# Kernel optimization log

Measured on AMD Instinct MI355X. Metric: run time of the kernel, lower is better.

The kernel has to match this reference:

```python
import jax, jax.numpy as jnp
import numpy as np

C = 256
CQK = C // 8  # query/key channels


def setup_inputs() -> dict:
    key = jax.random.key(0)
    ks = jax.random.split(key, 7)
    B, H, W = 4, 64, 64
    x = jax.random.normal(ks[0], (B, C, H, W), dtype=jnp.float32)
    # 1x1 conv weights stored as [out_ch, in_ch] (kernel spatial dims are 1)
    sc = 1.0 / np.sqrt(C)
    Wq = jax.random.uniform(ks[1], (CQK, C), jnp.float32, -sc, sc)
    bq = jax.random.uniform(ks[2], (CQK,), jnp.float32, -sc, sc)
    Wk = jax.random.uniform(ks[3], (CQK, C), jnp.float32, -sc, sc)
    bk = jax.random.uniform(ks[4], (CQK,), jnp.float32, -sc, sc)
    Wv = jax.random.uniform(ks[5], (C, C), jnp.float32, -sc, sc)
    bv = jax.random.uniform(ks[6], (C,), jnp.float32, -sc, sc)
    gamma = jnp.zeros((1,), dtype=jnp.float32)
    return {"x": x, "Wq": Wq, "bq": bq, "Wk": Wk, "bk": bk, "Wv": Wv, "bv": bv, "gamma": gamma}


def reference(x, Wq, bq, Wk, bk, Wv, bv, gamma):
    B, Ch, H, W = x.shape
    N = H * W
    xf = x.reshape(B, Ch, N)  # [B, C, N]
    # 1x1 convs == per-pixel linear projections
    q = jnp.einsum('oc,bcn->bno', Wq, xf) + bq  # [B, N, CQK]
    k = jnp.einsum('oc,bcn->bon', Wk, xf) + bk[None, :, None]  # [B, CQK, N]
    v = jnp.einsum('oc,bcn->bon', Wv, xf) + bv[None, :, None]  # [B, C, N]
    s = jnp.einsum('bnd,bdm->bnm', q, k)  # [B, N, N]
    attn = jax.nn.softmax(s, axis=-1)
    # out[b,c,i] = sum_j v[b,c,j] * attn[b,i,j]
    out = jnp.einsum('bcj,bij->bci', v, attn).reshape(B, Ch, H, W)
    return x + gamma[0] * out
```

## Files before the change

### kernel.cpp

```cpp
#include <hip/hip_runtime.h>
#include <math.h>

#define BATCH 4
#define CCH   256
#define DQK   32
#define NPIX  4096
#define LOG2E 1.44269504088896340736f

typedef __attribute__((ext_vector_type(8)))  short          short8_t;
typedef __attribute__((ext_vector_type(4)))  unsigned short ushort4_t;
typedef __attribute__((ext_vector_type(8)))  unsigned short ushort8_t;
typedef __attribute__((ext_vector_type(16))) float          f32x16;
typedef __attribute__((ext_vector_type(2)))  unsigned int   uint2_t;

#if __has_builtin(__builtin_amdgcn_exp2f)
#define EXP2F(x) __builtin_amdgcn_exp2f(x)
#else
#define EXP2F(x) exp2f(x)
#endif

#define MFMA32(a, b, c) __builtin_amdgcn_mfma_f32_32x32x16_bf16(a, b, c, 0, 0, 0)

static __device__ __forceinline__ unsigned short f2bf(float f) {
    union { float f; unsigned int u; } v; v.f = f;
    unsigned int r = v.u + 0x7FFFu + ((v.u >> 16) & 1u);
    return (unsigned short)(r >> 16);
}

static __device__ __forceinline__ short8_t cat8(ushort4_t a, ushort4_t b) {
    ushort8_t c = __builtin_shufflevector(a, b, 0, 1, 2, 3, 4, 5, 6, 7);
    short8_t r; __builtin_memcpy(&r, &c, 16); return r;
}

static __device__ __forceinline__ short8_t u4_to_s8(const unsigned int* u) {
    short8_t r; __builtin_memcpy(&r, u, 16); return r;
}

static __device__ __forceinline__ uint2_t plswap(unsigned int a, unsigned int b) {
#if __has_builtin(__builtin_amdgcn_permlane32_swap)
    return __builtin_amdgcn_permlane32_swap(a, b, false, false);
#else
    const unsigned int sa = (unsigned int)__shfl_xor((int)a, 32);
    const unsigned int sb = (unsigned int)__shfl_xor((int)b, 32);
    const int h = (threadIdx.x >> 5) & 1;
    uint2_t r;
    r.x = h ? sb : a;
    r.y = h ? b : sa;
    return r;
#endif
}

__global__ __launch_bounds__(256) void wconv_kernel(
    const float* __restrict__ Wq, const float* __restrict__ Wk,
    const float* __restrict__ Wv, unsigned short* __restrict__ wbf)
{
    const int idx = blockIdx.x * 256 + threadIdx.x;
    const int o = idx >> 8, c = idx & 255;
    float v;
    if (o < 32)      v = Wq[o * 256 + c] * LOG2E;
    else if (o < 64) v = Wk[(o - 32) * 256 + c];
    else             v = Wv[(o - 64) * 256 + c];
    wbf[((c >> 3) * 320 + o) * 8 + (c & 7)] = f2bf(v);
}

__global__ __launch_bounds__(320) void proj_kernel(
    const float* __restrict__ x, const unsigned short* __restrict__ wbf,
    const float* __restrict__ bq, const float* __restrict__ bk,
    const float* __restrict__ bv,
    unsigned short* __restrict__ q_bf, unsigned short* __restrict__ k_bf,
    unsigned short* __restrict__ v_bf)
{
    __shared__ unsigned short xs[32 * 256];
    const int b  = blockIdx.x >> 7;
    const int n0 = (blockIdx.x & 127) << 5;
    const int t  = threadIdx.x;

    if (t < 256) {
        const int px = t & 31, cg = t >> 5;
        const float* xp = x + ((size_t)b * CCH + cg * 32) * NPIX + n0 + px;
        unsigned short* row = xs + px * 256;
        const int sw = px & 15;
        #pragma unroll 4
        for (int cc = 0; cc < 32; cc += 2) {
            const float a0 = xp[(size_t)cc * NPIX];
            const float a1 = xp[(size_t)(cc + 1) * NPIX];
            const unsigned int pk = __builtin_amdgcn_perm(
                __float_as_uint(a1), __float_as_uint(a0), 0x07060302u);
            const int c = cg * 32 + cc;
            *(unsigned int*)&row[(((c >> 2) ^ sw) << 2) + (c & 3)] = pk;
        }
    }
    __syncthreads();

    const int w = t >> 6, lane = t & 63, il = lane & 31, h = lane >> 5;

    f32x16 acc0, acc1;
    #pragma unroll
    for (int r = 0; r < 16; ++r) { acc0[r] = 0.f; acc1[r] = 0.f; }

    const unsigned short* wp = wbf + ((size_t)(h * 320 + w * 64 + il)) * 8;
    const unsigned short* xrow = xs + il * 256;
    const int sw = il & 15;

    #pragma unroll 4
    for (int ks = 0; ks < 16; ++ks) {
        short8_t af0 = *(const short8_t*)(wp + ks * 5120);
        short8_t af1 = *(const short8_t*)(wp + ks * 5120 + 256);
        const int k0c = ks * 4 + h * 2;
        ushort4_t lo = *(const ushort4_t*)&xrow[((k0c    ) ^ sw) << 2];
        ushort4_t hi = *(const ushort4_t*)&xrow[((k0c + 1) ^ sw) << 2];
        short8_t bfr = cat8(lo, hi);
        acc0 = MFMA32(af0, bfr, acc0);
        acc1 = MFMA32(af1, bfr, acc1);
    }

    const int px = n0 + il;
    #pragma unroll
    for (int r = 0; r < 16; ++r) {
        const int orow = (r & 3) + 8 * (r >> 2) + 4 * h;
        if (w == 0) {
            q_bf[((size_t)(b * NPIX + px)) * 32 + orow] = f2bf(acc0[r] + bq[orow] * LOG2E);
            k_bf[((size_t)(b * NPIX + px)) * 32 + orow] = f2bf(acc1[r] + bk[orow]);
        } else {
            const int c0 = (w - 1) * 64 + orow;
            v_bf[((size_t)(b * CCH + c0))      * NPIX + px] = f2bf(acc0[r] + bv[c0]);
            v_bf[((size_t)(b * CCH + c0 + 32)) * NPIX + px] = f2bf(acc1[r] + bv[c0 + 32]);
        }
    }
}

#define RSTRIDE 40
#define KSZ     (64 * RSTRIDE)
#define BUFSZ   ((64 + 512) * RSTRIDE)

static __device__ __forceinline__ void make_bfrag(
    const f32x16& s, float& l0, float& l1, unsigned int bfr[2][4])
{
    float pv[16];
    #pragma unroll
    for (int r = 0; r < 16; ++r) pv[r] = EXP2F(s[r]);
    #pragma unroll
    for (int r = 0; r < 16; r += 2) { l0 += pv[r]; l1 += pv[r + 1]; }
    unsigned int P[8];
    #pragma unroll
    for (int v = 0; v < 8; ++v)
        P[v] = __builtin_amdgcn_perm(__float_as_uint(pv[2 * v + 1]),
                                     __float_as_uint(pv[2 * v]), 0x07060302u);
    #pragma unroll
    for (int kp = 0; kp < 2; ++kp) {
        const uint2_t r02 = plswap(P[4 * kp + 0], P[4 * kp + 2]);
        const uint2_t r13 = plswap(P[4 * kp + 1], P[4 * kp + 3]);
        bfr[kp][0] = r02.x; bfr[kp][1] = r13.x;
        bfr[kp][2] = r02.y; bfr[kp][3] = r13.y;
    }
}

__global__ __launch_bounds__(512) void attn_kernel(
    const unsigned short* __restrict__ qb,
    const unsigned short* __restrict__ kb,
    const unsigned short* __restrict__ vb,
    const float* __restrict__ x,
    const float* __restrict__ gamma,
    float* __restrict__ out)
{
    __shared__ unsigned short lds[BUFSZ];

    const int b  = blockIdx.x >> 6;
    const int i0 = (blockIdx.x & 63) << 6;
    const int t  = threadIdx.x;
    const int w = t >> 6, lane = t & 63, il = lane & 31, h = lane >> 5;
    const int ci = w & 3, jj = w >> 2;
    const int cbase = ci * 64;
    const int swz = (il >> 2) & 3;

    const unsigned short* vptr[4];
    int vofs[4];
    #pragma unroll
    for (int r = 0; r < 4; ++r) {
        const int u = r * 512 + t;
        const int c = u >> 3, jv = (u >> 2) & 1, q = u & 3;
        vptr[r] = vb + ((size_t)(b * CCH + c)) * NPIX + jv * 2048 + q * 8;
        vofs[r] = KSZ + (jv * 256 + c) * RSTRIDE + ((q ^ ((c >> 2) & 3)) << 3);
    }
    const int kr = t >> 2, kq = t & 3;
    const unsigned short* kptr = kb +
        ((size_t)(b * NPIX + (kr >> 5) * 2048 + (kr & 31))) * 32 + kq * 8;
    const int kofs = kr * RSTRIDE + ((kq ^ ((kr >> 2) & 3)) << 3);

    int kfo[2], vfo[2][2];
    #pragma unroll
    for (int ks = 0; ks < 2; ++ks)
        kfo[ks] = (jj * 32 + il) * RSTRIDE + (((ks * 2 + h) ^ swz) << 3);
    #pragma unroll
    for (int ct = 0; ct < 2; ++ct)
        #pragma unroll
        for (int kp = 0; kp < 2; ++kp)
            vfo[ct][kp] = KSZ + (jj * 256 + cbase + ct * 32 + il) * RSTRIDE +
                          (((kp * 2 + h) ^ swz) << 3);

    short8_t qf[2][2];
    #pragma unroll
    for (int it = 0; it < 2; ++it) {
        const unsigned short* qp = qb + ((size_t)(b * NPIX + i0 + it * 32 + il)) * 32 + h * 8;
        qf[it][0] = *(const short8_t*)qp;
        qf[it][1] = *(const short8_t*)(qp + 16);
    }

    f32x16 zf;
    #pragma unroll
    for (int r = 0; r < 16; ++r) zf[r] = 0.f;
    f32x16 acc[2][2];
    #pragma unroll
    for (int a = 0; a < 2; ++a)
        #pragma unroll
        for (int c2 = 0; c2 < 2; ++c2) acc[a][c2] = zf;
    float ls[2][2] = {{0.f, 0.f}, {0.f, 0.f}};

    short8_t vstg[4], kstg;
    #pragma unroll
    for (int r = 0; r < 4; ++r) vstg[r] = *(const short8_t*)(vptr[r]);
    if (t < 256) kstg = *(const short8_t*)(kptr);

    for (int jt = 0; jt < 64; ++jt) {
        if (jt > 0) __syncthreads();
        #pragma unroll
        for (int r = 0; r < 4; ++r) *(short8_t*)(lds + vofs[r]) = vstg[r];
        if (t < 256) *(short8_t*)(lds + kofs) = kstg;
        if (jt < 63) {
            #pragma unroll
            for (int r = 0; r < 4; ++r)
                vstg[r] = *(const short8_t*)(vptr[r] + (jt + 1) * 32);
            if (t < 256) kstg = *(const short8_t*)(kptr + (size_t)(jt + 1) * 1024);
        }
        __syncthreads();

        const short8_t kf0 = *(const short8_t*)(lds + kfo[0]);
        const short8_t kf1 = *(const short8_t*)(lds + kfo[1]);
        f32x16 s0 = MFMA32(kf0, qf[0][0], zf);
        s0 = MFMA32(kf1, qf[0][1], s0);
        f32x16 s1 = MFMA32(kf0, qf[1][0], zf);
        s1 = MFMA32(kf1, qf[1][1], s1);

        unsigned int bf0[2][4], bf1[2][4];
        make_bfrag(s0, ls[0][0], ls[0][1], bf0);
        make_bfrag(s1, ls[1][0], ls[1][1], bf1);

        const short8_t vf00 = *(const short8_t*)(lds + vfo[0][0]);
        const short8_t vf01 = *(const short8_t*)(lds + vfo[0][1]);
        const short8_t vf10 = *(const short8_t*)(lds + vfo[1][0]);
        const short8_t vf11 = *(const short8_t*)(lds + vfo[1][1]);

        acc[0][0] = MFMA32(vf00, u4_to_s8(bf0[0]), acc[0][0]);
        acc[0][0] = MFMA32(vf01, u4_to_s8(bf0[1]), acc[0][0]);
        acc[0][1] = MFMA32(vf10, u4_to_s8(bf0[0]), acc[0][1]);
        acc[0][1] = MFMA32(vf11, u4_to_s8(bf0[1]), acc[0][1]);
        acc[1][0] = MFMA32(vf00, u4_to_s8(bf1[0]), acc[1][0]);
        acc[1][0] = MFMA32(vf01, u4_to_s8(bf1[1]), acc[1][0]);
        acc[1][1] = MFMA32(vf10, u4_to_s8(bf1[0]), acc[1][1]);
        acc[1][1] = MFMA32(vf11, u4_to_s8(bf1[1]), acc[1][1]);
    }

    float l[2];
    #pragma unroll
    for (int it = 0; it < 2; ++it) {
        l[it] = ls[it][0] + ls[it][1];
        l[it] += __shfl_xor(l[it], 32);
    }
    const float gam = gamma[0];
    float* cf = (float*)lds;
    const int my = (w * 64 + lane) * 17;
    const int pb = ((w ^ 4) * 64 + lane) * 17;

    #pragma unroll
    for (int it = 0; it < 2; ++it) {
        __syncthreads();
        #pragma unroll
        for (int r = 0; r < 16; ++r)
            cf[my + r] = jj ? acc[it][0][r] : acc[it][1][r];
        cf[my + 16] = l[it];
        __syncthreads();
        const float lt = l[it] + cf[pb + 16];
        const float sc = gam / lt;
        #pragma unroll
        for (int r = 0; r < 16; ++r) {
            const float o = (jj ? acc[it][1][r] : acc[it][0][r]) + cf[pb + r];
            const int c = cbase + jj * 32 + (r & 3) + 8 * (r >> 2) + 4 * h;
            const size_t idx = ((size_t)(b * CCH + c)) * NPIX + i0 + it * 32 + il;
            out[idx] = x[idx] + o * sc;
        }
    }
}

extern "C" void kernel_launch(void* const* d_in, const int* in_sizes, int n_in,
                              void* d_out, int out_size, void* d_ws, size_t ws_size,
                              hipStream_t stream) {
    const float* x     = (const float*)d_in[0];
    const float* Wq    = (const float*)d_in[1];
    const float* bq    = (const float*)d_in[2];
    const float* Wk    = (const float*)d_in[3];
    const float* bk    = (const float*)d_in[4];
    const float* Wv    = (const float*)d_in[5];
    const float* bv    = (const float*)d_in[6];
    const float* gamma = (const float*)d_in[7];
    float* out = (float*)d_out;

    unsigned short* ws  = (unsigned short*)d_ws;
    unsigned short* wbf = ws;
    unsigned short* qbf = ws + 81920;
    unsigned short* kbf = qbf + (size_t)BATCH * NPIX * DQK;
    unsigned short* vbf = kbf + (size_t)BATCH * NPIX * DQK;

    wconv_kernel<<<dim3(320), dim3(256), 0, stream>>>(Wq, Wk, Wv, wbf);
    proj_kernel<<<dim3(BATCH * (NPIX / 32)), dim3(320), 0, stream>>>(
        x, wbf, bq, bk, bv, qbf, kbf, vbf);
    attn_kernel<<<dim3(BATCH * (NPIX / 64)), dim3(512), 0, stream>>>(
        qbf, kbf, vbf, x, gamma, out);
}
```

Measured before the change: 164.3 us.

## Pre-swizzle Q/K/V into MFMA fragment layout and stream directly from global memory

Adds a transpose kernel that writes x in bf16 MFMA-fragment order. The projection kernel now emits Q, K and V in fragment-ready layouts, staged through shared memory for coalesced stores. The attention kernel drops its shared-memory K/V staging and per-tile barriers, loading fragments straight from global memory with a two-stage register double buffer. Blocks are also remapped so each batch's tiles interleave across the grid for L2 sharing. The cost is one extra kernel launch and an extra pass over x, and the attention kernel now depends on L2 and cache hits for K/V reuse instead of explicit LDS sharing.

```diff
diff --git a/kernel.cpp b/kernel.cpp
--- a/kernel.cpp
+++ b/kernel.cpp
@@ -50,6 +50,28 @@
 #endif
 }
 
+static __device__ __forceinline__ void make_bfrag(
+    const f32x16& s, float& l0, float& l1, unsigned int bfr[2][4])
+{
+    float pv[16];
+    #pragma unroll
+    for (int r = 0; r < 16; ++r) pv[r] = EXP2F(s[r]);
+    #pragma unroll
+    for (int r = 0; r < 16; r += 2) { l0 += pv[r]; l1 += pv[r + 1]; }
+    unsigned int P[8];
+    #pragma unroll
+    for (int v = 0; v < 8; ++v)
+        P[v] = __builtin_amdgcn_perm(__float_as_uint(pv[2 * v + 1]),
+                                     __float_as_uint(pv[2 * v]), 0x07060302u);
+    #pragma unroll
+    for (int kp = 0; kp < 2; ++kp) {
+        const uint2_t r02 = plswap(P[4 * kp + 0], P[4 * kp + 2]);
+        const uint2_t r13 = plswap(P[4 * kp + 1], P[4 * kp + 3]);
+        bfr[kp][0] = r02.x; bfr[kp][1] = r13.x;
+        bfr[kp][2] = r02.y; bfr[kp][3] = r13.y;
+    }
+}
+
 __global__ __launch_bounds__(256) void wconv_kernel(
     const float* __restrict__ Wq, const float* __restrict__ Wk,
     const float* __restrict__ Wv, unsigned short* __restrict__ wbf)
@@ -63,148 +85,173 @@
     wbf[((c >> 3) * 320 + o) * 8 + (c & 7)] = f2bf(v);
 }
 
+__global__ __launch_bounds__(256) void xt_kernel(
+    const float* __restrict__ x, unsigned short* __restrict__ xfrag)
+{
+    const int b  = blockIdx.x >> 6;
+    const int cg = (blockIdx.x >> 4) & 3;
+    const int ng = blockIdx.x & 15;
+    const int t  = threadIdx.x;
+    const int w = t >> 6, l = t & 63;
+
+    #pragma unroll
+    for (int sgl = 0; sgl < 2; ++sgl) {
+        const int sg = w * 2 + sgl;
+        float f[4][8];
+        #pragma unroll
+        for (int p = 0; p < 8; ++p) {
+            const float* row = x + ((size_t)(b * CCH + cg * 64 + sg * 8 + p)) * NPIX
+                                 + ng * 256;
+            #pragma unroll
+            for (int j = 0; j < 4; ++j)
+                f[j][p] = row[j * 64 + l];
+        }
+        #pragma unroll
+        for (int j = 0; j < 4; ++j) {
+            unsigned int d[4];
+            #pragma unroll
+            for (int k = 0; k < 4; ++k)
+                d[k] = __builtin_amdgcn_perm(__float_as_uint(f[j][2 * k + 1]),
+                                             __float_as_uint(f[j][2 * k]), 0x07060302u);
+            const int nt = ng * 8 + j * 2 + (l >> 5);
+            unsigned short* dst = xfrag +
+                ((((size_t)(b * 128 + nt) * 32) + cg * 8 + sg) * 32 + (l & 31)) * 8;
+            *(short8_t*)dst = u4_to_s8(d);
+        }
+    }
+}
+
 __global__ __launch_bounds__(320) void proj_kernel(
-    const float* __restrict__ x, const unsigned short* __restrict__ wbf,
+    const unsigned short* __restrict__ xfrag, const unsigned short* __restrict__ wbf,
     const float* __restrict__ bq, const float* __restrict__ bk,
     const float* __restrict__ bv,
-    unsigned short* __restrict__ q_bf, unsigned short* __restrict__ k_bf,
-    unsigned short* __restrict__ v_bf)
-{
-    __shared__ unsigned short xs[32 * 256];
-    const int b  = blockIdx.x >> 7;
-    const int n0 = (blockIdx.x & 127) << 5;
-    const int t  = threadIdx.x;
-
-    if (t < 256) {
-        const int px = t & 31, cg = t >> 5;
-        const float* xp = x + ((size_t)b * CCH + cg * 32) * NPIX + n0 + px;
-        unsigned short* row = xs + px * 256;
-        const int sw = px & 15;
-        #pragma unroll 4
-        for (int cc = 0; cc < 32; cc += 2) {
-            const float a0 = xp[(size_t)cc * NPIX];
-            const float a1 = xp[(size_t)(cc + 1) * NPIX];
-            const unsigned int pk = __builtin_amdgcn_perm(
-                __float_as_uint(a1), __float_as_uint(a0), 0x07060302u);
-            const int c = cg * 32 + cc;
-            *(unsigned int*)&row[(((c >> 2) ^ sw) << 2) + (c & 3)] = pk;
-        }
-    }
-    __syncthreads();
-
+    unsigned short* __restrict__ qfrag, unsigned short* __restrict__ kfrag,
+    unsigned short* __restrict__ vfrag)
+{
+    __shared__ unsigned short qkb[2 * 2 * 32 * 40];
+    __shared__ unsigned short vbuf[4 * 64 * 72];
+
+    const int b   = blockIdx.x >> 6;
+    const int nt0 = (blockIdx.x & 63) << 1;
+    const int t   = threadIdx.x;
     const int w = t >> 6, lane = t & 63, il = lane & 31, h = lane >> 5;
 
-    f32x16 acc0, acc1;
-    #pragma unroll
-    for (int r = 0; r < 16; ++r) { acc0[r] = 0.f; acc1[r] = 0.f; }
+    float4 bA[4], bB[4];
+    #pragma unroll
+    for (int g = 0; g < 4; ++g) {
+        if (w == 0) {
+            bA[g] = *(const float4*)&bq[8 * g + 4 * h];
+            bB[g] = *(const float4*)&bk[8 * g + 4 * h];
+        } else {
+            bA[g] = *(const float4*)&bv[(w - 1) * 64 + 8 * g + 4 * h];
+            bB[g] = *(const float4*)&bv[(w - 1) * 64 + 32 + 8 * g + 4 * h];
+        }
+    }
+
+    f32x16 acc[2][2];
+    #pragma unroll
+    for (int a = 0; a < 2; ++a)
+        #pragma unroll
+        for (int i = 0; i < 2; ++i)
+            #pragma unroll
+            for (int r = 0; r < 16; ++r) acc[a][i][r] = 0.f;
 
     const unsigned short* wp = wbf + ((size_t)(h * 320 + w * 64 + il)) * 8;
-    const unsigned short* xrow = xs + il * 256;
-    const int sw = il & 15;
+    const unsigned short* xp0 = xfrag + (((size_t)(b * 128 + nt0) * 32 + h) * 32 + il) * 8;
+    const unsigned short* xp1 = xp0 + (size_t)32 * 32 * 8;
 
     #pragma unroll 4
     for (int ks = 0; ks < 16; ++ks) {
-        short8_t af0 = *(const short8_t*)(wp + ks * 5120);
-        short8_t af1 = *(const short8_t*)(wp + ks * 5120 + 256);
-        const int k0c = ks * 4 + h * 2;
-        ushort4_t lo = *(const ushort4_t*)&xrow[((k0c    ) ^ sw) << 2];
-        ushort4_t hi = *(const ushort4_t*)&xrow[((k0c + 1) ^ sw) << 2];
-        short8_t bfr = cat8(lo, hi);
-        acc0 = MFMA32(af0, bfr, acc0);
-        acc1 = MFMA32(af1, bfr, acc1);
-    }
-
-    const int px = n0 + il;
-    #pragma unroll
-    for (int r = 0; r < 16; ++r) {
-        const int orow = (r & 3) + 8 * (r >> 2) + 4 * h;
-        if (w == 0) {
-            q_bf[((size_t)(b * NPIX + px)) * 32 + orow] = f2bf(acc0[r] + bq[orow] * LOG2E);
-            k_bf[((size_t)(b * NPIX + px)) * 32 + orow] = f2bf(acc1[r] + bk[orow]);
-        } else {
-            const int c0 = (w - 1) * 64 + orow;
-            v_bf[((size_t)(b * CCH + c0))      * NPIX + px] = f2bf(acc0[r] + bv[c0]);
-            v_bf[((size_t)(b * CCH + c0 + 32)) * NPIX + px] = f2bf(acc1[r] + bv[c0 + 32]);
-        }
-    }
-}
-
-#define RSTRIDE 40
-#define KSZ     (64 * RSTRIDE)
-#define BUFSZ   ((64 + 512) * RSTRIDE)
-
-static __device__ __forceinline__ void make_bfrag(
-    const f32x16& s, float& l0, float& l1, unsigned int bfr[2][4])
-{
-    float pv[16];
-    #pragma unroll
-    for (int r = 0; r < 16; ++r) pv[r] = EXP2F(s[r]);
-    #pragma unroll
-    for (int r = 0; r < 16; r += 2) { l0 += pv[r]; l1 += pv[r + 1]; }
-    unsigned int P[8];
-    #pragma unroll
-    for (int v = 0; v < 8; ++v)
-        P[v] = __builtin_amdgcn_perm(__float_as_uint(pv[2 * v + 1]),
-                                     __float_as_uint(pv[2 * v]), 0x07060302u);
-    #pragma unroll
-    for (int kp = 0; kp < 2; ++kp) {
-        const uint2_t r02 = plswap(P[4 * kp + 0], P[4 * kp + 2]);
-        const uint2_t r13 = plswap(P[4 * kp + 1], P[4 * kp + 3]);
-        bfr[kp][0] = r02.x; bfr[kp][1] = r13.x;
-        bfr[kp][2] = r02.y; bfr[kp][3] = r13.y;
-    }
-}
+        const short8_t af0 = *(const short8_t*)(wp + ks * 5120);
+        const short8_t af1 = *(const short8_t*)(wp + ks * 5120 + 256);
+        const short8_t bf0 = *(const short8_t*)(xp0 + (size_t)ks * 2 * 256);
+        const short8_t bf1 = *(const short8_t*)(xp1 + (size_t)ks * 2 * 256);
+        acc[0][0] = MFMA32(af0, bf0, acc[0][0]);
+        acc[0][1] = MFMA32(af0, bf1, acc[0][1]);
+        acc[1][0] = MFMA32(af1, bf0, acc[1][0]);
+        acc[1][1] = MFMA32(af1, bf1, acc[1][1]);
+    }
+
+    if (w == 0) {
+        #pragma unroll
+        for (int it = 0; it < 2; ++it)
+            #pragma unroll
+            for (int r = 0; r < 16; ++r) {
+                const int d = (r & 3) + 8 * (r >> 2) + 4 * h;
+                qkb[(it * 2 + 0) * 1280 + il * 40 + d] =
+                    f2bf(acc[0][it][r] + bA[r >> 2][r & 3] * LOG2E);
+                qkb[(it * 2 + 1) * 1280 + il * 40 + d] =
+                    f2bf(acc[1][it][r] + bB[r >> 2][r & 3]);
+            }
+        #pragma unroll
+        for (int it = 0; it < 2; ++it)
+            #pragma unroll
+            for (int rep = 0; rep < 2; ++rep) {
+                const int u = rep * 64 + lane;
+                const int slot = u >> 5, n = u & 31;
+                ushort4_t qlo = *(const ushort4_t*)&qkb[(it * 2) * 1280 + n * 40 + slot * 8];
+                ushort4_t qhi = *(const ushort4_t*)&qkb[(it * 2) * 1280 + n * 40 + slot * 8 + 4];
+                ushort4_t klo = *(const ushort4_t*)&qkb[(it * 2 + 1) * 1280 + n * 40 + slot * 8];
+                ushort4_t khi = *(const ushort4_t*)&qkb[(it * 2 + 1) * 1280 + n * 40 + slot * 8 + 4];
+                const size_t o8 = (((size_t)(b * 128 + nt0 + it) * 4 + slot) * 32 + n) * 8;
+                *(short8_t*)(qfrag + o8) = cat8(qlo, qhi);
+                *(short8_t*)(kfrag + o8) = cat8(klo, khi);
+            }
+    } else {
+        unsigned short* vb = vbuf + (w - 1) * 64 * 72;
+        #pragma unroll
+        for (int it = 0; it < 2; ++it)
+            #pragma unroll
+            for (int r = 0; r < 16; ++r) {
+                const int orow = (r & 3) + 8 * (r >> 2) + 4 * h;
+                vb[(orow)      * 72 + it * 32 + il] = f2bf(acc[0][it][r] + bA[r >> 2][r & 3]);
+                vb[(orow + 32) * 72 + it * 32 + il] = f2bf(acc[1][it][r] + bB[r >> 2][r & 3]);
+            }
+        #pragma unroll
+        for (int rep = 0; rep < 8; ++rep) {
+            const int u = rep * 64 + lane;
+            const int c = u & 63, m = u >> 6;
+            const int it = m >> 2, slot = m & 3;
+            ushort4_t lo = *(const ushort4_t*)&vb[c * 72 + it * 32 + slot * 8];
+            ushort4_t hi = *(const ushort4_t*)&vb[c * 72 + it * 32 + slot * 8 + 4];
+            const size_t o8 = (((size_t)(b * 128 + nt0 + it) * 4 + slot) * 256 +
+                               (w - 1) * 64 + c) * 8;
+            *(short8_t*)(vfrag + o8) = cat8(lo, hi);
+        }
+    }
+}
+
+struct Stage { short8_t k0, k1, v00, v01, v10, v11; };
 
 __global__ __launch_bounds__(512) void attn_kernel(
-    const unsigned short* __restrict__ qb,
-    const unsigned short* __restrict__ kb,
-    const unsigned short* __restrict__ vb,
+    const unsigned short* __restrict__ qfrag,
+    const unsigned short* __restrict__ kfrag,
+    const unsigned short* __restrict__ vfrag,
     const float* __restrict__ x,
     const float* __restrict__ gamma,
     float* __restrict__ out)
 {
-    __shared__ unsigned short lds[BUFSZ];
-
-    const int b  = blockIdx.x >> 6;
-    const int i0 = (blockIdx.x & 63) << 6;
+    __shared__ float comb[8][64][17];
+
+    const int m8 = blockIdx.x & 7;
+    const int b  = m8 >> 1;
+    const int itile = ((blockIdx.x >> 3) << 1) | (m8 & 1);
+    const int i0 = itile << 6;
     const int t  = threadIdx.x;
     const int w = t >> 6, lane = t & 63, il = lane & 31, h = lane >> 5;
     const int ci = w & 3, jj = w >> 2;
     const int cbase = ci * 64;
-    const int swz = (il >> 2) & 3;
-
-    const unsigned short* vptr[4];
-    int vofs[4];
-    #pragma unroll
-    for (int r = 0; r < 4; ++r) {
-        const int u = r * 512 + t;
-        const int c = u >> 3, jv = (u >> 2) & 1, q = u & 3;
-        vptr[r] = vb + ((size_t)(b * CCH + c)) * NPIX + jv * 2048 + q * 8;
-        vofs[r] = KSZ + (jv * 256 + c) * RSTRIDE + ((q ^ ((c >> 2) & 3)) << 3);
-    }
-    const int kr = t >> 2, kq = t & 3;
-    const unsigned short* kptr = kb +
-        ((size_t)(b * NPIX + (kr >> 5) * 2048 + (kr & 31))) * 32 + kq * 8;
-    const int kofs = kr * RSTRIDE + ((kq ^ ((kr >> 2) & 3)) << 3);
-
-    int kfo[2], vfo[2][2];
-    #pragma unroll
-    for (int ks = 0; ks < 2; ++ks)
-        kfo[ks] = (jj * 32 + il) * RSTRIDE + (((ks * 2 + h) ^ swz) << 3);
-    #pragma unroll
-    for (int ct = 0; ct < 2; ++ct)
-        #pragma unroll
-        for (int kp = 0; kp < 2; ++kp)
-            vfo[ct][kp] = KSZ + (jj * 256 + cbase + ct * 32 + il) * RSTRIDE +
-                          (((kp * 2 + h) ^ swz) << 3);
 
     short8_t qf[2][2];
     #pragma unroll
-    for (int it = 0; it < 2; ++it) {
-        const unsigned short* qp = qb + ((size_t)(b * NPIX + i0 + it * 32 + il)) * 32 + h * 8;
-        qf[it][0] = *(const short8_t*)qp;
-        qf[it][1] = *(const short8_t*)(qp + 16);
-    }
+    for (int it = 0; it < 2; ++it)
+        #pragma unroll
+        for (int ks = 0; ks < 2; ++ks)
+            qf[it][ks] = *(const short8_t*)(qfrag +
+                (((size_t)(b * 128 + itile * 2 + it) * 4 + ks * 2 + h) * 32 + il) * 8);
+
+    const size_t kbase = (size_t)(b * 128 + jj * 64) * 1024 + h * 256 + il * 8;
+    const size_t vbase = (size_t)(b * 128 + jj * 64) * 8192 + h * 2048 + (cbase + il) * 8;
 
     f32x16 zf;
     #pragma unroll
@@ -216,48 +263,42 @@
         for (int c2 = 0; c2 < 2; ++c2) acc[a][c2] = zf;
     float ls[2][2] = {{0.f, 0.f}, {0.f, 0.f}};
 
-    short8_t vstg[4], kstg;
-    #pragma unroll
-    for (int r = 0; r < 4; ++r) vstg[r] = *(const short8_t*)(vptr[r]);
-    if (t < 256) kstg = *(const short8_t*)(kptr);
-
-    for (int jt = 0; jt < 64; ++jt) {
-        if (jt > 0) __syncthreads();
-        #pragma unroll
-        for (int r = 0; r < 4; ++r) *(short8_t*)(lds + vofs[r]) = vstg[r];
-        if (t < 256) *(short8_t*)(lds + kofs) = kstg;
-        if (jt < 63) {
-            #pragma unroll
-            for (int r = 0; r < 4; ++r)
-                vstg[r] = *(const short8_t*)(vptr[r] + (jt + 1) * 32);
-            if (t < 256) kstg = *(const short8_t*)(kptr + (size_t)(jt + 1) * 1024);
-        }
-        __syncthreads();
-
-        const short8_t kf0 = *(const short8_t*)(lds + kfo[0]);
-        const short8_t kf1 = *(const short8_t*)(lds + kfo[1]);
-        f32x16 s0 = MFMA32(kf0, qf[0][0], zf);
-        s0 = MFMA32(kf1, qf[0][1], s0);
-        f32x16 s1 = MFMA32(kf0, qf[1][0], zf);
-        s1 = MFMA32(kf1, qf[1][1], s1);
-
+    Stage A, B;
+    auto load = [&](Stage& S, int jt) {
+        const unsigned short* kp = kfrag + kbase + (size_t)jt * 1024;
+        S.k0  = *(const short8_t*)kp;
+        S.k1  = *(const short8_t*)(kp + 512);
+        const unsigned short* vp = vfrag + vbase + (size_t)jt * 8192;
+        S.v00 = *(const short8_t*)vp;
+        S.v01 = *(const short8_t*)(vp + 4096);
+        S.v10 = *(const short8_t*)(vp + 256);
+        S.v11 = *(const short8_t*)(vp + 4352);
+    };
+    auto compute = [&](const Stage& S) {
+        f32x16 s0 = MFMA32(S.k0, qf[0][0], zf);
+        s0 = MFMA32(S.k1, qf[0][1], s0);
+        f32x16 s1 = MFMA32(S.k0, qf[1][0], zf);
+        s1 = MFMA32(S.k1, qf[1][1], s1);
         unsigned int bf0[2][4], bf1[2][4];
         make_bfrag(s0, ls[0][0], ls[0][1], bf0);
         make_bfrag(s1, ls[1][0], ls[1][1], bf1);
-
-        const short8_t vf00 = *(const short8_t*)(lds + vfo[0][0]);
-        const short8_t vf01 = *(const short8_t*)(lds + vfo[0][1]);
-        const short8_t vf10 = *(const short8_t*)(lds + vfo[1][0]);
-        const short8_t vf11 = *(const short8_t*)(lds + vfo[1][1]);
-
-        acc[0][0] = MFMA32(vf00, u4_to_s8(bf0[0]), acc[0][0]);
-        acc[0][0] = MFMA32(vf01, u4_to_s8(bf0[1]), acc[0][0]);
-        acc[0][1] = MFMA32(vf10, u4_to_s8(bf0[0]), acc[0][1]);
-        acc[0][1] = MFMA32(vf11, u4_to_s8(bf0[1]), acc[0][1]);
-        acc[1][0] = MFMA32(vf00, u4_to_s8(bf1[0]), acc[1][0]);
-        acc[1][0] = MFMA32(vf01, u4_to_s8(bf1[1]), acc[1][0]);
-        acc[1][1] = MFMA32(vf10, u4_to_s8(bf1[0]), acc[1][1]);
-        acc[1][1] = MFMA32(vf11, u4_to_s8(bf1[1]), acc[1][1]);
+        acc[0][0] = MFMA32(S.v00, u4_to_s8(bf0[0]), acc[0][0]);
+        acc[0][0] = MFMA32(S.v01, u4_to_s8(bf0[1]), acc[0][0]);
+        acc[0][1] = MFMA32(S.v10, u4_to_s8(bf0[0]), acc[0][1]);
+        acc[0][1] = MFMA32(S.v11, u4_to_s8(bf0[1]), acc[0][1]);
+        acc[1][0] = MFMA32(S.v00, u4_to_s8(bf1[0]), acc[1][0]);
+        acc[1][0] = MFMA32(S.v01, u4_to_s8(bf1[1]), acc[1][0]);
+        acc[1][1] = MFMA32(S.v10, u4_to_s8(bf1[0]), acc[1][1]);
+        acc[1][1] = MFMA32(S.v11, u4_to_s8(bf1[1]), acc[1][1]);
+    };
+
+    load(A, 0);
+    load(B, 1);
+    for (int jt = 0; jt < 64; jt += 2) {
+        compute(A);
+        if (jt + 2 < 64) load(A, jt + 2);
+        compute(B);
+        if (jt + 3 < 64) load(B, jt + 3);
     }
 
     float l[2];
@@ -267,23 +308,21 @@
         l[it] += __shfl_xor(l[it], 32);
     }
     const float gam = gamma[0];
-    float* cf = (float*)lds;
-    const int my = (w * 64 + lane) * 17;
-    const int pb = ((w ^ 4) * 64 + lane) * 17;
 
     #pragma unroll
     for (int it = 0; it < 2; ++it) {
         __syncthreads();
         #pragma unroll
         for (int r = 0; r < 16; ++r)
-            cf[my + r] = jj ? acc[it][0][r] : acc[it][1][r];
-        cf[my + 16] = l[it];
+            comb[w][lane][r] = jj ? acc[it][0][r] : acc[it][1][r];
+        comb[w][lane][16] = l[it];
         __syncthreads();
-        const float lt = l[it] + cf[pb + 16];
+        const int pw = w ^ 4;
+        const float lt = l[it] + comb[pw][lane][16];
         const float sc = gam / lt;
         #pragma unroll
         for (int r = 0; r < 16; ++r) {
-            const float o = (jj ? acc[it][1][r] : acc[it][0][r]) + cf[pb + r];
+            const float o = (jj ? acc[it][1][r] : acc[it][0][r]) + comb[pw][lane][r];
             const int c = cbase + jj * 32 + (r & 3) + 8 * (r >> 2) + 4 * h;
             const size_t idx = ((size_t)(b * CCH + c)) * NPIX + i0 + it * 32 + il;
             out[idx] = x[idx] + o * sc;
@@ -304,15 +343,17 @@
     const float* gamma = (const float*)d_in[7];
     float* out = (float*)d_out;
 
-    unsigned short* ws  = (unsigned short*)d_ws;
-    unsigned short* wbf = ws;
-    unsigned short* qbf = ws + 81920;
-    unsigned short* kbf = qbf + (size_t)BATCH * NPIX * DQK;
-    unsigned short* vbf = kbf + (size_t)BATCH * NPIX * DQK;
+    unsigned short* ws    = (unsigned short*)d_ws;
+    unsigned short* wbf   = ws;
+    unsigned short* xfrag = ws + 81920;
+    unsigned short* qfrag = xfrag + (size_t)4194304;
+    unsigned short* kfrag = qfrag + (size_t)524288;
+    unsigned short* vfrag = kfrag + (size_t)524288;
 
     wconv_kernel<<<dim3(320), dim3(256), 0, stream>>>(Wq, Wk, Wv, wbf);
-    proj_kernel<<<dim3(BATCH * (NPIX / 32)), dim3(320), 0, stream>>>(
-        x, wbf, bq, bk, bv, qbf, kbf, vbf);
-    attn_kernel<<<dim3(BATCH * (NPIX / 64)), dim3(512), 0, stream>>>(
-        qbf, kbf, vbf, x, gamma, out);
-}
+    xt_kernel<<<dim3(256), dim3(256), 0, stream>>>(x, xfrag);
+    proj_kernel<<<dim3(256), dim3(320), 0, stream>>>(
+        xfrag, wbf, bq, bk, bv, qfrag, kfrag, vfrag);
+    attn_kernel<<<dim3(256), dim3(512), 0, stream>>>(
+        qfrag, kfrag, vfrag, x, gamma, out);
+}
```

Result: faster. 154.2 us (-6.2%).
